# Performance work log

Hardware: AMD Instinct MI355X
Metric: run time of the kernel (lower is better)

The kernel has to match this reference:

```python
import jax, jax.numpy as jnp
import numpy as np

D = 64      # embedding_dim
GD = 8      # ground_dim
NV = 8192   # num variables (batch_size=1 * max_variables)
NC = 32768  # num clauses


def setup_inputs() -> dict:
    key = jax.random.key(0)
    ks = jax.random.split(key, 24)
    s = 1.0 / np.sqrt(D)
    sg = 1.0 / np.sqrt(GD + D)
    lin = lambda k, shp, sc: (jax.random.uniform(k, shp, jnp.float32) * 2 - 1) * sc
    inp = {
        'variables': jax.random.normal(ks[0], (1, NV, D), jnp.float32),
        'ground_vars': jax.random.normal(ks[1], (NV, GD), jnp.float32),
        # sparse 0/1 incidence matrices stored densely (as the torch code does)
        'cmat_pos': jax.random.bernoulli(ks[2], 0.02, (NC, NV)).astype(jnp.float32),
        'cmat_neg': jax.random.bernoulli(ks[3], 0.02, (NC, NV)).astype(jnp.float32),
        'v_mat': jnp.zeros((1,), jnp.float32),   # overwritten in forward; dummy
        'c_mat': jnp.zeros((1,), jnp.float32),   # overwritten in forward; dummy
        # parameters
        'fb_block': jax.random.normal(ks[4], (2, D, D), jnp.float32),  # nn_init.normal_
        'vb': jax.random.normal(ks[5], (D,), jnp.float32),
        'cb': jax.random.normal(ks[6], (D,), jnp.float32),
        # ground combiner: Linear(GD + D -> D) followed by tanh
        'Wg': lin(ks[7], (D, GD + D), sg), 'bg': lin(ks[8], (D,), sg),
        # GRU operator weights (W_*: no bias, U_*: with bias since gru_bias=True)
        'Wz': lin(ks[9], (D, D), s), 'Uz': lin(ks[10], (D, D), s), 'bz': lin(ks[11], (D,), s),
        'Wr': lin(ks[12], (D, D), s), 'Ur': lin(ks[13], (D, D), s), 'br': lin(ks[14], (D,), s),
        'Wh': lin(ks[15], (D, D), s), 'Uh': lin(ks[16], (D, D), s), 'bh': lin(ks[17], (D,), s),
    }
    return inp


def reference(variables, ground_vars, cmat_pos, cmat_neg, v_mat, c_mat,
              fb_block, vb, cb, Wg, bg, Wz, Uz, bz, Wr, Ur, br, Wh, Uh, bh):
    d = variables.shape[-1]
    v = variables.reshape(-1, d)                      # [NV, D]
    cm = cmat_pos - cmat_neg                          # signed incidence [NC, NV]
    # variable -> clause message: mm(fb[0], v.T).T == v @ fb[0].T
    vars_fwd = v @ fb_block[0].T                      # [NV, D]
    c = jax.nn.relu(cm @ vars_fwd + cb)               # [NC, D]
    # clause -> variable message via transposed incidence
    nv = cm.T @ (c @ fb_block[1].T)                   # [NV, D]
    v_emb = jax.nn.relu(nv + vb)
    # ground combiner: tanh(Linear(concat([ground, emb])))
    v_emb = jnp.tanh(jnp.concatenate([ground_vars, v_emb], axis=-1) @ Wg.T + bg)
    # GRU update against previous embeddings
    prev = v
    z = jax.nn.sigmoid(v_emb @ Wz.T + prev @ Uz.T + bz)
    r = jax.nn.sigmoid(v_emb @ Wr.T + prev @ Ur.T + br)
    h_tilda = jnp.tanh(v_emb @ Wh.T + (r * prev) @ Uh.T + bh)
    new_vars = (1 - z) * prev + z * h_tilda           # [NV, D]
    return new_vars.reshape(1, NV * d, 1)             # rc view
```

## Files before the change

### kernel.cpp

```cpp
#include <hip/hip_runtime.h>
#include <stdint.h>

typedef unsigned long long u64;
typedef float f32x4 __attribute__((ext_vector_type(4)));

#define NVAR 8192
#define NCLS 32768
#define CSEG 16
#define GSEG 4
#define LCAP 1152

__device__ __forceinline__ float lane_bc(float v, int l) { return __shfl(v, l); }

__device__ __forceinline__ u64 readfl64(u64 x) {
  unsigned lo = __builtin_amdgcn_readfirstlane((unsigned)x);
  unsigned hi = __builtin_amdgcn_readfirstlane((unsigned)(x >> 32));
  return ((u64)hi << 32) | (u64)lo;
}

__device__ __forceinline__ u64 shflx64(u64 x, int m) {
  unsigned lo = (unsigned)__shfl_xor((int)(unsigned)x, m, 64);
  unsigned hi = (unsigned)__shfl_xor((int)(unsigned)(x >> 32), m, 64);
  return ((u64)hi << 32) | (u64)lo;
}

__global__ __launch_bounds__(256) void k_varsfwd(const float* __restrict__ v,
                                                 const float* __restrict__ fb0,
                                                 float* __restrict__ out) {
  __shared__ float fbt[64 * 64];
  __shared__ float vrow[4][64];
  int t = threadIdx.x;
#pragma unroll
  for (int i = 0; i < 16; ++i) {
    int idx = i * 256 + t;
    fbt[(idx & 63) * 64 + (idx >> 6)] = fb0[idx];
  }
  __syncthreads();
  int w = t >> 6, lane = t & 63;
  for (int rr = 0; rr < 16; rr += 4) {
    int row = blockIdx.x * 16 + rr + w;
    vrow[w][lane] = v[row * 64 + lane];
    __syncthreads();
    double a = 0.0;
#pragma unroll
    for (int k = 0; k < 64; ++k)
      a = fma((double)vrow[w][k], (double)fbt[k * 64 + lane], a);
    out[row * 64 + lane] = (float)a;
    __syncthreads();
  }
}

__global__ __launch_bounds__(512, 8) void k_pass1v7(
    const float* __restrict__ pos, const float* __restrict__ neg,
    const float* __restrict__ vfwd, const float* __restrict__ fb1,
    const float* __restrict__ cbias, float* __restrict__ dmat,
    u64* __restrict__ vbs) {
  __shared__ float sbuf[128 * 64];
  __shared__ u64 lm[2][32][4];
  __shared__ u64 lsg[2][32][4];
  int t = threadIdx.x;
  int w = __builtin_amdgcn_readfirstlane(t >> 6);
  int lane = t & 63;
  int orig = blockIdx.x;
  int bx = ((orig & 7) << 7) + (orig >> 3);
  int c0 = bx * 32;
  int cb = bx >> 1;
  int h = bx & 1;
  double acc[4];
#pragma unroll
  for (int i = 0; i < 4; ++i) acc[i] = 0.0;

  for (int g = 0; g < 32; ++g) {
    int par = g & 1;
    const float4* s0 = (const float4*)(vfwd + (size_t)g * 256 * 64);
    float4 st0 = s0[t], st1 = s0[t + 512], st2 = s0[t + 1024], st3 = s0[t + 1536];
#pragma unroll
    for (int i = 0; i < 4; i += 2) {
      size_t rb0 = (size_t)(c0 + w * 4 + i) * 2048 + (size_t)g * 64 + lane;
      size_t rb1 = rb0 + 2048;
      f32x4 p0 = __builtin_nontemporal_load(&((const f32x4*)pos)[rb0]);
      f32x4 q0 = __builtin_nontemporal_load(&((const f32x4*)neg)[rb0]);
      f32x4 p1 = __builtin_nontemporal_load(&((const f32x4*)pos)[rb1]);
      f32x4 q1 = __builtin_nontemporal_load(&((const f32x4*)neg)[rb1]);
      f32x4 a0 = p0 - q0;
      f32x4 a1 = p1 - q1;
      int cl0 = w * 4 + i, cl1 = cl0 + 1;
#pragma unroll
      for (int j = 0; j < 4; ++j) {
        u64 m = __ballot(a0[j] != 0.f);
        u64 sg = __ballot(a0[j] < 0.f);
        if (lane == j) { lm[par][cl0][j] = m; lsg[par][cl0][j] = sg; }
      }
#pragma unroll
      for (int j = 0; j < 4; ++j) {
        u64 m = __ballot(a1[j] != 0.f);
        u64 sg = __ballot(a1[j] < 0.f);
        if (lane == j) { lm[par][cl1][j] = m; lsg[par][cl1][j] = sg; }
      }
    }
    __syncthreads();

    {
      float4* dst = (float4*)sbuf;
      dst[t] = st0; dst[t + 512] = st1; dst[t + 1024] = st2; dst[t + 1536] = st3;
    }
    if (w < 4) {
      int jw = w;
      u64 A = (lane < 32) ? lm[par][lane][jw] : lsg[par][lane - 32][jw];
#define BSTEP(J, M)                                          \
      {                                                      \
        u64 B = shflx64(A, J);                               \
        u64 keep = (lane & J) ? ~(u64)(M) : (u64)(M);        \
        u64 B2 = (lane & J) ? (B >> J) : (B << J);           \
        A = (A & keep) | (B2 & ~keep);                       \
      }
      BSTEP(32, 0x00000000FFFFFFFFULL)
      BSTEP(16, 0x0000FFFF0000FFFFULL)
      BSTEP(8,  0x00FF00FF00FF00FFULL)
      BSTEP(4,  0x0F0F0F0F0F0F0F0FULL)
      BSTEP(2,  0x3333333333333333ULL)
      BSTEP(1,  0x5555555555555555ULL)
#undef BSTEP
      int v = (g << 8) + (lane << 2) + jw;
      vbs[((size_t)v * 512 + cb) * 2 + h] = A;
    }
    __syncthreads();

    const float4* s1 = s0 + 2048;
    st0 = s1[t]; st1 = s1[t + 512]; st2 = s1[t + 1024]; st3 = s1[t + 1536];
#pragma unroll
    for (int i = 0; i < 4; ++i) {
      int cl = w * 4 + i;
#pragma unroll
      for (int j = 0; j < 4; ++j) {
        u64 m = readfl64(lm[par][cl][j]) & 0xffffffffULL;
        u64 sg = readfl64(lsg[par][cl][j]);
        while (m) {
          int l = __builtin_ctzll(m);
          m &= m - 1;
          float dv = sbuf[(l * 4 + j) * 64 + lane];
          acc[i] += ((sg >> l) & 1) ? -(double)dv : (double)dv;
        }
      }
    }
    __syncthreads();

    {
      float4* dst = (float4*)sbuf;
      dst[t] = st0; dst[t + 512] = st1; dst[t + 1024] = st2; dst[t + 1536] = st3;
    }
    __syncthreads();

#pragma unroll
    for (int i = 0; i < 4; ++i) {
      int cl = w * 4 + i;
#pragma unroll
      for (int j = 0; j < 4; ++j) {
        u64 m = readfl64(lm[par][cl][j]) >> 32;
        u64 sg = readfl64(lsg[par][cl][j]) >> 32;
        while (m) {
          int l = __builtin_ctzll(m);
          m &= m - 1;
          float dv = sbuf[(l * 4 + j) * 64 + lane];
          acc[i] += ((sg >> l) & 1) ? -(double)dv : (double)dv;
        }
      }
    }
  }
  __syncthreads();

#pragma unroll
  for (int i2 = 0; i2 < 8; ++i2) {
    int idx = i2 * 512 + t;
    sbuf[(idx & 63) * 64 + (idx >> 6)] = fb1[idx];
  }
  float* crow = sbuf + 4096 + w * 64;
  __syncthreads();
  for (int i = 0; i < 4; ++i) {
    float cv = fmaxf((float)acc[i] + cbias[lane], 0.f);
    crow[lane] = cv;
    __syncthreads();
    double da = 0.0;
#pragma unroll
    for (int k = 0; k < 64; ++k)
      da = fma((double)crow[k], (double)sbuf[k * 64 + lane], da);
    dmat[(size_t)(c0 + w * 4 + i) * 64 + lane] = (float)da;
    __syncthreads();
  }
}

__global__ __launch_bounds__(256, 8) void k_gather4(const u64* __restrict__ vbs,
                                                    const float* __restrict__ dmat,
                                                    double* __restrict__ nvd4) {
  __shared__ __align__(16) unsigned short list[4][LCAP];
  int w = __builtin_amdgcn_readfirstlane(threadIdx.x >> 6);
  int lane = threadIdx.x & 63;
  int seg = blockIdx.x >> 11;
  int v = (blockIdx.x & 2047) * 4 + w;
  int cc0 = seg * (512 / GSEG);
  const u64* P = vbs + ((size_t)v * 512 + cc0) * 2;
  u64 a0 = P[lane * 4 + 0], a1 = P[lane * 4 + 1];
  u64 b0 = P[lane * 4 + 2], b1 = P[lane * 4 + 3];
  u64 m0 = (a0 & 0xffffffffULL) | (a1 << 32);
  u64 s0 = (a0 >> 32) | (a1 & 0xffffffff00000000ULL);
  u64 m1 = (b0 & 0xffffffffULL) | (b1 << 32);
  u64 s1 = (b0 >> 32) | (b1 & 0xffffffff00000000ULL);
  int cnt = __popcll(m0) + __popcll(m1);
  int pre = cnt;
#pragma unroll
  for (int d = 1; d < 64; d <<= 1) {
    int o = __shfl_up(pre, d, 64);
    if (lane >= d) pre += o;
  }
  int tot = __shfl(pre, 63, 64);
  int base = pre - cnt;
#pragma unroll
  for (int half = 0; half < 2; ++half) {
    u64 m = half ? m1 : m0;
    u64 s = half ? s1 : s0;
    int cbase = (cc0 + 2 * lane + half) * 64;
    while (m) {
      int b = __builtin_ctzll(m);
      m &= m - 1;
      if (base < LCAP)
        list[w][base] = (unsigned short)((cbase + b) | (((s >> b) & 1) << 15));
      ++base;
    }
  }
  __syncthreads();
  if (tot > LCAP) tot = LCAP;
  const u64* lp = (const u64*)&list[w][0];
  double acc = 0.0;
  int k = 0;
  for (; k + 8 <= tot; k += 8) {
    u64 L0 = lp[k >> 2], L1 = lp[(k >> 2) + 1];
    unsigned e[8];
#pragma unroll
    for (int q = 0; q < 4; ++q) {
      e[q] = (unsigned)(L0 >> (16 * q)) & 0xffffu;
      e[4 + q] = (unsigned)(L1 >> (16 * q)) & 0xffffu;
    }
    float dv[8];
#pragma unroll
    for (int q = 0; q < 8; ++q)
      dv[q] = dmat[(size_t)(e[q] & 0x7fffu) * 64 + lane];
#pragma unroll
    for (int q = 0; q < 8; ++q)
      acc += (e[q] & 0x8000u) ? -(double)dv[q] : (double)dv[q];
  }
  for (; k < tot; ++k) {
    unsigned e = list[w][k];
    float dv = dmat[(size_t)(e & 0x7fffu) * 64 + lane];
    acc += (e & 0x8000u) ? -(double)dv : (double)dv;
  }
  nvd4[((size_t)seg * NVAR + v) * 64 + lane] = acc;
}

__global__ __launch_bounds__(256) void k_pass1_basic(
    const float* __restrict__ pos, const float* __restrict__ neg,
    const float* __restrict__ bmat, const float* __restrict__ fb1,
    const float* __restrict__ cbias, float* __restrict__ dmat) {
  __shared__ float fbt[64 * 64];
  __shared__ float crow[4][64];
  int t = threadIdx.x;
#pragma unroll
  for (int i = 0; i < 16; ++i) {
    int idx = i * 256 + t;
    fbt[(idx & 63) * 64 + (idx >> 6)] = fb1[idx];
  }
  __syncthreads();
  int w = t >> 6, lane = t & 63;
  int c = blockIdx.x * 4 + w;
  const float4* prow = (const float4*)(pos + (size_t)c * NVAR);
  const float4* nrow = (const float4*)(neg + (size_t)c * NVAR);
  double acc = 0.0;
  for (int g = 0; g < 32; ++g) {
    float4 p = prow[g * 64 + lane];
    float4 q = nrow[g * 64 + lane];
    float sc[4];
    sc[0] = p.x - q.x; sc[1] = p.y - q.y; sc[2] = p.z - q.z; sc[3] = p.w - q.w;
#pragma unroll
    for (int j = 0; j < 4; ++j) {
      float s = sc[j];
      u64 m = __ballot(s != 0.f);
      u64 sg = __ballot(s < 0.f);
      while (m) {
        int l = __builtin_ctzll(m);
        m &= m - 1;
        float dv = bmat[(size_t)((g << 8) + (l << 2) + j) * 64 + lane];
        acc += ((sg >> l) & 1) ? -(double)dv : (double)dv;
      }
    }
  }
  float cv = fmaxf((float)acc + cbias[lane], 0.f);
  crow[w][lane] = cv;
  __syncthreads();
  double da = 0.0;
#pragma unroll
  for (int k = 0; k < 64; ++k)
    da = fma((double)crow[w][k], (double)fbt[k * 64 + lane], da);
  dmat[(size_t)c * 64 + lane] = (float)da;
}

__global__ __launch_bounds__(256) void k_pass2_dense(
    const float* __restrict__ pos, const float* __restrict__ neg,
    const float* __restrict__ dmat, double* __restrict__ nvd4) {
  __shared__ float acc[64 * 64];
  int t = threadIdx.x;
#pragma unroll
  for (int i = 0; i < 16; ++i) acc[i * 256 + t] = 0.f;
  __syncthreads();
  int w = t >> 6, lane = t & 63;
  int s = blockIdx.x / CSEG, seg = blockIdx.x % CSEG;
  int c0 = seg * (NCLS / CSEG);
  for (int c = c0 + w; c < c0 + NCLS / CSEG; c += 4) {
    float p = pos[(size_t)c * NVAR + (s << 6) + lane];
    float q = neg[(size_t)c * NVAR + (s << 6) + lane];
    float sv = p - q;
    u64 m = __ballot(sv != 0.f);
    if (!m) continue;
    float dv = dmat[(size_t)c * 64 + lane];
    while (m) {
      int l = __builtin_ctzll(m);
      m &= m - 1;
      float sl = lane_bc(sv, l);
      atomicAdd(&acc[(l << 6) + lane], sl * dv);
    }
  }
  __syncthreads();
  size_t obase = (size_t)s * 4096;
#pragma unroll
  for (int i = 0; i < 16; ++i) {
    int idx = i * 256 + t;
    atomicAdd(&nvd4[obase + idx], (double)acc[idx]);
  }
}

__global__ __launch_bounds__(256, 1) void k_tailfused(
    const double* __restrict__ nvd4, const float* __restrict__ vb,
    const float* __restrict__ ground, const float* __restrict__ Wg,
    const float* __restrict__ bg,
    const float* __restrict__ Wz, const float* __restrict__ Uz,
    const float* __restrict__ bz,
    const float* __restrict__ Wr, const float* __restrict__ Ur,
    const float* __restrict__ br,
    const float* __restrict__ Wh, const float* __restrict__ Uh,
    const float* __restrict__ bh,
    const float* __restrict__ prev, float* __restrict__ out) {
  __shared__ float wg[72 * 65];
  __shared__ float wz[64 * 65], uz[64 * 65], wr[64 * 65], ur[64 * 65],
      wh[64 * 65], uh[64 * 65];
  __shared__ float xrow[4][72], yrow[4][64], prow[4][64], rprow[4][64];
  int t = threadIdx.x;
#pragma unroll
  for (int i = 0; i < 18; ++i) {
    int idx = i * 256 + t;
    wg[(idx % 72) * 65 + (idx / 72)] = Wg[idx];
  }
#pragma unroll
  for (int i = 0; i < 16; ++i) {
    int idx = i * 256 + t;
    int a = (idx & 63) * 65 + (idx >> 6);
    wz[a] = Wz[idx]; uz[a] = Uz[idx]; wr[a] = Wr[idx];
    ur[a] = Ur[idx]; wh[a] = Wh[idx]; uh[a] = Uh[idx];
  }
  __syncthreads();
  int w = t >> 6, lane = t & 63;
  const size_t SS = (size_t)NVAR * 64;
  for (int rr = 0; rr < 8; ++rr) {
    int row = blockIdx.x * 32 + w * 8 + rr;
    size_t ix = (size_t)row * 64 + lane;
    float pv = prev[ix];
    double nv = (nvd4[ix] + nvd4[SS + ix]) + (nvd4[2 * SS + ix] + nvd4[3 * SS + ix]);
    float ve = fmaxf((float)nv + vb[lane], 0.f);
    xrow[w][8 + lane] = ve;
    if (lane < 8) xrow[w][lane] = ground[row * 8 + lane];
    prow[w][lane] = pv;
    double a = 0.0;
#pragma unroll
    for (int k = 0; k < 72; ++k)
      a = fma((double)xrow[w][k], (double)wg[k * 65 + lane], a);
    float ve2 = tanhf((float)a + bg[lane]);
    yrow[w][lane] = ve2;
    float az = bz[lane], ar = br[lane];
#pragma unroll
    for (int k = 0; k < 64; ++k) {
      float y = yrow[w][k], p = prow[w][k];
      az = fmaf(y, wz[k * 65 + lane], az);
      az = fmaf(p, uz[k * 65 + lane], az);
      ar = fmaf(y, wr[k * 65 + lane], ar);
      ar = fmaf(p, ur[k * 65 + lane], ar);
    }
    float r = 1.f / (1.f + expf(-ar));
    rprow[w][lane] = r * pv;
    float ah = bh[lane];
#pragma unroll
    for (int k = 0; k < 64; ++k) {
      ah = fmaf(yrow[w][k], wh[k * 65 + lane], ah);
      ah = fmaf(rprow[w][k], uh[k * 65 + lane], ah);
    }
    float z = 1.f / (1.f + expf(-az));
    float hh = tanhf(ah);
    out[ix] = (1.f - z) * pv + z * hh;
  }
}

extern "C" void kernel_launch(void* const* d_in, const int* in_sizes, int n_in,
                              void* d_out, int out_size, void* d_ws, size_t ws_size,
                              hipStream_t stream) {
  const float* variables = (const float*)d_in[0];
  const float* ground    = (const float*)d_in[1];
  const float* cpos      = (const float*)d_in[2];
  const float* cneg      = (const float*)d_in[3];
  const float* fb        = (const float*)d_in[6];
  const float* vb        = (const float*)d_in[7];
  const float* cb        = (const float*)d_in[8];
  const float* Wg        = (const float*)d_in[9];
  const float* bg        = (const float*)d_in[10];
  const float* Wz        = (const float*)d_in[11];
  const float* Uz        = (const float*)d_in[12];
  const float* bz        = (const float*)d_in[13];
  const float* Wr        = (const float*)d_in[14];
  const float* Ur        = (const float*)d_in[15];
  const float* br        = (const float*)d_in[16];
  const float* Wh        = (const float*)d_in[17];
  const float* Uh        = (const float*)d_in[18];
  const float* bh        = (const float*)d_in[19];
  float* out = (float*)d_out;
  char* ws = (char*)d_ws;
  const size_t MB = (size_t)1 << 20;

  float* vfwd   = (float*)(ws + 0);
  float* dmat   = (float*)(ws + 2 * MB);
  double* nvd4  = (double*)(ws + 10 * MB);
  u64* vbs      = (u64*)(ws + 26 * MB);
  bool fast = ws_size >= 96 * MB;

  k_varsfwd<<<512, 256, 0, stream>>>(variables, fb, vfwd);
  if (fast) {
    k_pass1v7<<<1024, 512, 0, stream>>>(cpos, cneg, vfwd, fb + 4096, cb, dmat,
                                        vbs);
    k_gather4<<<2048 * GSEG, 256, 0, stream>>>(vbs, dmat, nvd4);
  } else {
    (void)hipMemsetAsync(nvd4, 0, (size_t)GSEG * NVAR * 64 * sizeof(double),
                         stream);
    k_pass1_basic<<<8192, 256, 0, stream>>>(cpos, cneg, vfwd, fb + 4096, cb, dmat);
    k_pass2_dense<<<128 * CSEG, 256, 0, stream>>>(cpos, cneg, dmat, nvd4);
  }
  k_tailfused<<<256, 256, 0, stream>>>(nvd4, vb, ground, Wg, bg, Wz, Uz, bz,
                                       Wr, Ur, br, Wh, Uh, bh, variables, out);
}
```

Measured before the change: 755.8 us.

## Split clause pass into mask streaming kernel and list-based clause gather kernel

The fused pass that streamed the incidence matrices and gathered vfwd rows through LDS is split in two. The first kernel only streams pos/neg, builds ballot bitmasks and writes both the transposed per-variable masks and a new per-clause mask buffer. A second kernel builds a compacted per-clause index list with a prefix scan, gathers vfwd rows straight from global memory, and applies relu plus the fb1 projection. The aim is to keep the streaming kernel purely bandwidth-bound and stop it stalling on the sparse gather, at the cost of writing and re-reading a 64MB mask buffer. It also adds a list cap of 512 entries per clause and raises the workspace requirement for the fast path.

```diff
diff --git a/kernel.cpp b/kernel.cpp
--- a/kernel.cpp
+++ b/kernel.cpp
@@ -9,6 +9,7 @@
 #define CSEG 16
 #define GSEG 4
 #define LCAP 1152
+#define LC2  512
 
 __device__ __forceinline__ float lane_bc(float v, int l) { return __shfl(v, l); }
 
@@ -50,12 +51,9 @@
   }
 }
 
-__global__ __launch_bounds__(512, 8) void k_pass1v7(
+__global__ __launch_bounds__(512, 8) void k_stream(
     const float* __restrict__ pos, const float* __restrict__ neg,
-    const float* __restrict__ vfwd, const float* __restrict__ fb1,
-    const float* __restrict__ cbias, float* __restrict__ dmat,
-    u64* __restrict__ vbs) {
-  __shared__ float sbuf[128 * 64];
+    u64* __restrict__ cmask, u64* __restrict__ vbs) {
   __shared__ u64 lm[2][32][4];
   __shared__ u64 lsg[2][32][4];
   int t = threadIdx.x;
@@ -66,14 +64,9 @@
   int c0 = bx * 32;
   int cb = bx >> 1;
   int h = bx & 1;
-  double acc[4];
-#pragma unroll
-  for (int i = 0; i < 4; ++i) acc[i] = 0.0;
 
   for (int g = 0; g < 32; ++g) {
     int par = g & 1;
-    const float4* s0 = (const float4*)(vfwd + (size_t)g * 256 * 64);
-    float4 st0 = s0[t], st1 = s0[t + 512], st2 = s0[t + 1024], st3 = s0[t + 1536];
 #pragma unroll
     for (int i = 0; i < 4; i += 2) {
       size_t rb0 = (size_t)(c0 + w * 4 + i) * 2048 + (size_t)g * 64 + lane;
@@ -89,21 +82,25 @@
       for (int j = 0; j < 4; ++j) {
         u64 m = __ballot(a0[j] != 0.f);
         u64 sg = __ballot(a0[j] < 0.f);
-        if (lane == j) { lm[par][cl0][j] = m; lsg[par][cl0][j] = sg; }
+        if (lane == j) {
+          lm[par][cl0][j] = m; lsg[par][cl0][j] = sg;
+          size_t ci = ((size_t)(c0 + cl0) * 128 + (g << 2) + j) * 2;
+          cmask[ci] = m; cmask[ci + 1] = sg;
+        }
       }
 #pragma unroll
       for (int j = 0; j < 4; ++j) {
         u64 m = __ballot(a1[j] != 0.f);
         u64 sg = __ballot(a1[j] < 0.f);
-        if (lane == j) { lm[par][cl1][j] = m; lsg[par][cl1][j] = sg; }
+        if (lane == j) {
+          lm[par][cl1][j] = m; lsg[par][cl1][j] = sg;
+          size_t ci = ((size_t)(c0 + cl1) * 128 + (g << 2) + j) * 2;
+          cmask[ci] = m; cmask[ci + 1] = sg;
+        }
       }
     }
     __syncthreads();
 
-    {
-      float4* dst = (float4*)sbuf;
-      dst[t] = st0; dst[t + 512] = st1; dst[t + 1024] = st2; dst[t + 1536] = st3;
-    }
     if (w < 4) {
       int jw = w;
       u64 A = (lane < 32) ? lm[par][lane][jw] : lsg[par][lane - 32][jw];
@@ -124,69 +121,85 @@
       int v = (g << 8) + (lane << 2) + jw;
       vbs[((size_t)v * 512 + cb) * 2 + h] = A;
     }
-    __syncthreads();
-
-    const float4* s1 = s0 + 2048;
-    st0 = s1[t]; st1 = s1[t + 512]; st2 = s1[t + 1024]; st3 = s1[t + 1536];
-#pragma unroll
-    for (int i = 0; i < 4; ++i) {
-      int cl = w * 4 + i;
-#pragma unroll
-      for (int j = 0; j < 4; ++j) {
-        u64 m = readfl64(lm[par][cl][j]) & 0xffffffffULL;
-        u64 sg = readfl64(lsg[par][cl][j]);
-        while (m) {
-          int l = __builtin_ctzll(m);
-          m &= m - 1;
-          float dv = sbuf[(l * 4 + j) * 64 + lane];
-          acc[i] += ((sg >> l) & 1) ? -(double)dv : (double)dv;
-        }
-      }
-    }
-    __syncthreads();
-
-    {
-      float4* dst = (float4*)sbuf;
-      dst[t] = st0; dst[t + 512] = st1; dst[t + 1024] = st2; dst[t + 1536] = st3;
-    }
-    __syncthreads();
-
-#pragma unroll
-    for (int i = 0; i < 4; ++i) {
-      int cl = w * 4 + i;
-#pragma unroll
-      for (int j = 0; j < 4; ++j) {
-        u64 m = readfl64(lm[par][cl][j]) >> 32;
-        u64 sg = readfl64(lsg[par][cl][j]) >> 32;
-        while (m) {
-          int l = __builtin_ctzll(m);
-          m &= m - 1;
-          float dv = sbuf[(l * 4 + j) * 64 + lane];
-          acc[i] += ((sg >> l) & 1) ? -(double)dv : (double)dv;
-        }
-      }
-    }
-  }
-  __syncthreads();
-
-#pragma unroll
-  for (int i2 = 0; i2 < 8; ++i2) {
-    int idx = i2 * 512 + t;
-    sbuf[(idx & 63) * 64 + (idx >> 6)] = fb1[idx];
-  }
-  float* crow = sbuf + 4096 + w * 64;
-  __syncthreads();
-  for (int i = 0; i < 4; ++i) {
-    float cv = fmaxf((float)acc[i] + cbias[lane], 0.f);
-    crow[lane] = cv;
-    __syncthreads();
-    double da = 0.0;
-#pragma unroll
-    for (int k = 0; k < 64; ++k)
-      da = fma((double)crow[k], (double)sbuf[k * 64 + lane], da);
-    dmat[(size_t)(c0 + w * 4 + i) * 64 + lane] = (float)da;
-    __syncthreads();
-  }
+  }
+}
+
+__global__ __launch_bounds__(256, 8) void k_cgather(
+    const u64* __restrict__ cmask, const float* __restrict__ vfwd,
+    const float* __restrict__ fb1, const float* __restrict__ cbias,
+    float* __restrict__ dmat) {
+  __shared__ __align__(16) unsigned short list[4][LC2];
+  __shared__ float fbt[64 * 64];
+  __shared__ float crow[4][64];
+  int t = threadIdx.x;
+  int w = __builtin_amdgcn_readfirstlane(t >> 6);
+  int lane = t & 63;
+#pragma unroll
+  for (int i = 0; i < 16; ++i) {
+    int idx = i * 256 + t;
+    fbt[(idx & 63) * 64 + (idx >> 6)] = fb1[idx];
+  }
+  int cl = blockIdx.x * 4 + w;
+  const u64* P = cmask + (size_t)cl * 256;
+  u64 m0 = P[lane * 4 + 0], s0 = P[lane * 4 + 1];
+  u64 m1 = P[lane * 4 + 2], s1 = P[lane * 4 + 3];
+  int cnt = __popcll(m0) + __popcll(m1);
+  int pre = cnt;
+#pragma unroll
+  for (int d = 1; d < 64; d <<= 1) {
+    int o = __shfl_up(pre, d, 64);
+    if (lane >= d) pre += o;
+  }
+  int tot = __shfl(pre, 63, 64);
+  int base = pre - cnt;
+#pragma unroll
+  for (int half = 0; half < 2; ++half) {
+    u64 m = half ? m1 : m0;
+    u64 s = half ? s1 : s0;
+    int cc = 2 * lane + half;
+    int vb0 = (cc >> 2) * 256 + (cc & 3);
+    while (m) {
+      int b = __builtin_ctzll(m);
+      m &= m - 1;
+      if (base < LC2)
+        list[w][base] =
+            (unsigned short)((vb0 + (b << 2)) | (((s >> b) & 1) << 15));
+      ++base;
+    }
+  }
+  __syncthreads();
+  if (tot > LC2) tot = LC2;
+  const u64* lp = (const u64*)&list[w][0];
+  double acc = 0.0;
+  int k = 0;
+  for (; k + 8 <= tot; k += 8) {
+    u64 L0 = lp[k >> 2], L1 = lp[(k >> 2) + 1];
+    unsigned e[8];
+#pragma unroll
+    for (int q = 0; q < 4; ++q) {
+      e[q] = (unsigned)(L0 >> (16 * q)) & 0xffffu;
+      e[4 + q] = (unsigned)(L1 >> (16 * q)) & 0xffffu;
+    }
+    float dv[8];
+#pragma unroll
+    for (int q = 0; q < 8; ++q)
+      dv[q] = vfwd[(size_t)(e[q] & 0x1fffu) * 64 + lane];
+#pragma unroll
+    for (int q = 0; q < 8; ++q)
+      acc += (e[q] & 0x8000u) ? -(double)dv[q] : (double)dv[q];
+  }
+  for (; k < tot; ++k) {
+    unsigned e = list[w][k];
+    float dv = vfwd[(size_t)(e & 0x1fffu) * 64 + lane];
+    acc += (e & 0x8000u) ? -(double)dv : (double)dv;
+  }
+  float cv = fmaxf((float)acc + cbias[lane], 0.f);
+  crow[w][lane] = cv;
+  double da = 0.0;
+#pragma unroll
+  for (int k2 = 0; k2 < 64; ++k2)
+    da = fma((double)crow[w][k2], (double)fbt[k2 * 64 + lane], da);
+  dmat[(size_t)cl * 64 + lane] = (float)da;
 }
 
 __global__ __launch_bounds__(256, 8) void k_gather4(const u64* __restrict__ vbs,
@@ -434,12 +447,13 @@
   float* dmat   = (float*)(ws + 2 * MB);
   double* nvd4  = (double*)(ws + 10 * MB);
   u64* vbs      = (u64*)(ws + 26 * MB);
-  bool fast = ws_size >= 96 * MB;
+  u64* cmask    = (u64*)(ws + 90 * MB);
+  bool fast = ws_size >= 160 * MB;
 
   k_varsfwd<<<512, 256, 0, stream>>>(variables, fb, vfwd);
   if (fast) {
-    k_pass1v7<<<1024, 512, 0, stream>>>(cpos, cneg, vfwd, fb + 4096, cb, dmat,
-                                        vbs);
+    k_stream<<<1024, 512, 0, stream>>>(cpos, cneg, cmask, vbs);
+    k_cgather<<<NCLS / 4, 256, 0, stream>>>(cmask, vfwd, fb + 4096, cb, dmat);
     k_gather4<<<2048 * GSEG, 256, 0, stream>>>(vbs, dmat, nvd4);
   } else {
     (void)hipMemsetAsync(nvd4, 0, (size_t)GSEG * NVAR * 64 * sizeof(double),
```

Result: slower. 850.3 us (+12.5%).
